# Optimization experiments

Hardware: AMD Instinct MI355X
Metric: run time of the kernel (lower is better)

Reference implementation:

```python
import jax, jax.numpy as jnp
import numpy as np

B, S, D = 1, 2048, 2048
H = 16            # num query heads
QL = 1536         # q_lora_rank
KVL = 512         # kv_lora_rank
DN = 128          # qk_nope_head_dim
DR = 64           # qk_rope_head_dim
DV = 128          # v_head_dim
F = 8192          # ffn intermediate
EPS = 1e-6
WAVE = 10000.0


def _rms(x, scale, eps=EPS):
    # fp32 norm then cast back, matching DeepSeekV3_1RMSNorm
    x32 = x.astype(jnp.float32)
    ms = jnp.mean(x32 * x32, axis=-1, keepdims=True)
    return (x32 * jax.lax.rsqrt(ms + eps)).astype(x.dtype) * scale


def _rope_tables(seq_len, dim):
    inv_freq = 1.0 / (WAVE ** (jnp.arange(0, dim, 2, dtype=jnp.float32) / dim))
    t = jnp.arange(seq_len, dtype=jnp.float32)[:, None] * inv_freq[None, :]  # [S, dim/2]
    emb = jnp.concatenate([t, t], axis=-1)  # [S, dim]
    return jnp.cos(emb), jnp.sin(emb)


def _apply_rope(x, cos, sin):
    # x: [B, S, H, dr]; rotate-half convention
    half = x.shape[-1] // 2
    x1, x2 = x[..., :half], x[..., half:]
    rot = jnp.concatenate([-x2, x1], axis=-1)
    return x * cos[None, :, None, :] + rot * sin[None, :, None, :]


def setup_inputs() -> dict:
    key = jax.random.key(0)
    ks = jax.random.split(key, 12)
    w = lambda k, shp: (jax.random.normal(k, shp, dtype=jnp.float32) * 0.02)
    inp = {
        "hidden_states": jax.random.normal(ks[0], (B, S, D), dtype=jnp.float32),
        "attention_mask": jnp.broadcast_to(jnp.tril(jnp.ones((S, S), dtype=bool)), (B, S, S)),
        "pre_attn_scale": jnp.ones((D,), jnp.float32),
        "wqa": w(ks[1], (D, QL)),
        "q_norm_scale": jnp.ones((QL,), jnp.float32),
        "wqb": w(ks[2], (QL, H * (DN + DR))),
        "wkva": w(ks[3], (D, KVL + DR)),
        "kv_norm_scale": jnp.ones((KVL,), jnp.float32),
        "wkvb": w(ks[4], (KVL, H * (DN + DV))),
        "wo": w(ks[5], (H * DV, D)),
        "pre_ffn_scale": jnp.ones((D,), jnp.float32),
        "wg": w(ks[6], (D, F)),
        "bg": jnp.zeros((F,), jnp.float32),
        "wu": w(ks[7], (D, F)),
        "bu": jnp.zeros((F,), jnp.float32),
        "wd": w(ks[8], (F, D)),
        "bd": jnp.zeros((D,), jnp.float32),
    }
    return inp


def reference(hidden_states, attention_mask, pre_attn_scale, wqa, q_norm_scale, wqb,
              wkva, kv_norm_scale, wkvb, wo, pre_ffn_scale, wg, bg, wu, bu, wd, bd):
    x = hidden_states
    # --- pre-attention RMSNorm ---
    n = _rms(x, pre_attn_scale)
    # --- MLA attention ---
    q = (_rms(n @ wqa, q_norm_scale) @ wqb).reshape(B, S, H, DN + DR)
    q_nope, q_rope = q[..., :DN], q[..., DN:]
    kva = n @ wkva                              # [B,S,KVL+DR]
    c_kv, k_rope = kva[..., :KVL], kva[..., KVL:]
    kv = (_rms(c_kv, kv_norm_scale) @ wkvb).reshape(B, S, H, DN + DV)
    k_nope, v = kv[..., :DN], kv[..., DN:]
    cos, sin = _rope_tables(S, DR)
    q_rope = _apply_rope(q_rope, cos, sin)
    k_rope = _apply_rope(k_rope[:, :, None, :], cos, sin)  # [B,S,1,DR] shared across heads
    qf = jnp.concatenate([q_nope, q_rope], axis=-1)
    kf = jnp.concatenate([k_nope, jnp.broadcast_to(k_rope, (B, S, H, DR))], axis=-1)
    scale = 1.0 / float(np.sqrt(DN + DR))
    scores = jnp.einsum('bqhd,bkhd->bhqk', qf, kf) * scale
    scores = jnp.where(attention_mask[:, None, :, :], scores, jnp.float32(-1e9))
    probs = jax.nn.softmax(scores, axis=-1)
    attn = jnp.einsum('bhqk,bkhd->bqhd', probs, v).reshape(B, S, H * DV)
    x = x + attn @ wo                            # residual 1 (dropout=0)
    # --- pre-FFN RMSNorm + dense SwiGLU FFN ---
    n = _rms(x, pre_ffn_scale)
    ff = (jax.nn.silu(n @ wg + bg) * (n @ wu + bu)) @ wd + bd
    return x + ff                                # residual 2
```

## Files before the change

kernel.cpp:

```cpp
#include <hip/hip_runtime.h>
#include <hip/hip_bf16.h>
#include <stdint.h>

typedef unsigned short u16;
using f32x4  = __attribute__((ext_vector_type(4))) float;
using bf16x8 = __attribute__((ext_vector_type(8))) __bf16;
using u32x4  = __attribute__((ext_vector_type(4))) uint32_t;
using u16x4  = __attribute__((ext_vector_type(4))) unsigned short;
using u16x8  = __attribute__((ext_vector_type(8))) unsigned short;

#define S_LEN 2048
#define DM    2048
#define NH    16
#define QLR   1536
#define KVLR  512
#define DNOPE 128
#define DROPE 64
#define DVAL  128
#define FFD   8192

static __device__ __forceinline__ float bf2f(u16 u) {
    union { uint32_t i; float f; } v; v.i = ((uint32_t)u) << 16; return v.f;
}
static __device__ __forceinline__ u16 f2bf(float f) {
    union { float f; uint32_t i; } v; v.f = f;
    uint32_t x = v.i;
    return (u16)((x + 0x7FFF + ((x >> 16) & 1)) >> 16);
}
static __device__ __forceinline__ void gload16(const u16* g, const u16* l) {
    __builtin_amdgcn_global_load_lds(
        (const __attribute__((address_space(1))) void*)g,
        (__attribute__((address_space(3))) void*)l, 16, 0, 0);
}

__global__ __launch_bounds__(256)
void transpose_w(const float* __restrict__ src, u16* __restrict__ dst, int R, int C)
{
    __shared__ __align__(16) u16 tile[64][68];
    const int c0 = blockIdx.x * 64, r0 = blockIdx.y * 64;
    const int t = threadIdx.x;
#pragma unroll
    for (int i = 0; i < 4; ++i) {
        int idx = i * 256 + t;
        int r = idx >> 4, c4 = idx & 15;
        float4 v = *reinterpret_cast<const float4*>(&src[(size_t)(r0 + r) * C + c0 + c4 * 4]);
        u16x4 b; b[0] = f2bf(v.x); b[1] = f2bf(v.y); b[2] = f2bf(v.z); b[3] = f2bf(v.w);
        *reinterpret_cast<u16x4*>(&tile[r][c4 * 4]) = b;
    }
    __syncthreads();
#pragma unroll
    for (int i = 0; i < 4; ++i) {
        int idx = i * 256 + t;
        int rr = idx >> 4, k4 = idx & 15;
        u16x4 o;
#pragma unroll
        for (int j = 0; j < 4; ++j) o[j] = tile[k4 * 4 + j][rr];
        *reinterpret_cast<u16x4*>(&dst[(size_t)(c0 + rr) * R + r0 + k4 * 4]) = o;
    }
}

__global__ __launch_bounds__(256)
void transpose_v(const u16* __restrict__ kv, u16* __restrict__ vt)
{
    __shared__ __align__(16) u16 tile[64][76];
    const int t = threadIdx.x;
    const int s0 = blockIdx.x * 64;
    const int d0 = blockIdx.y * 64;
    const int h  = blockIdx.z;
#pragma unroll
    for (int i = 0; i < 2; ++i) {
        int idx = i * 256 + t;
        int s = idx >> 3, c8 = idx & 7;
        u16x8 v = *reinterpret_cast<const u16x8*>(kv + (size_t)(s0 + s) * (NH * 256) + h * 256 + 128 + d0 + c8 * 8);
        u16x4 lo, hi;
#pragma unroll
        for (int j = 0; j < 4; ++j) { lo[j] = v[j]; hi[j] = v[4 + j]; }
        *reinterpret_cast<u16x4*>(&tile[s][c8 * 8])     = lo;
        *reinterpret_cast<u16x4*>(&tile[s][c8 * 8 + 4]) = hi;
    }
    __syncthreads();
#pragma unroll
    for (int i = 0; i < 4; ++i) {
        int idx = i * 256 + t;
        int d = idx >> 4, s4 = idx & 15;
        u16x4 o;
#pragma unroll
        for (int j = 0; j < 4; ++j) o[j] = tile[s4 * 4 + j][d];
        *reinterpret_cast<u16x4*>(&vt[(size_t)(h * 128 + d0 + d) * S_LEN + s0 + s4 * 4]) = o;
    }
}

template<bool IN_F32>
__global__ __launch_bounds__(256)
void rms_norm(const void* __restrict__ in, int in_stride, int width,
              const float* __restrict__ scale, u16* __restrict__ out, int out_stride)
{
    const int row = blockIdx.x;
    const int t = threadIdx.x;
    const float* inf = (const float*)in;
    const u16*   inb = (const u16*)in;
    float ss = 0.f;
    for (int c = t; c < width; c += 256) {
        float v = IN_F32 ? inf[(size_t)row * in_stride + c] : bf2f(inb[(size_t)row * in_stride + c]);
        ss += v * v;
    }
#pragma unroll
    for (int o = 32; o > 0; o >>= 1) ss += __shfl_xor(ss, o);
    __shared__ float red[4];
    if ((t & 63) == 0) red[t >> 6] = ss;
    __syncthreads();
    float inv = rsqrtf((red[0] + red[1] + red[2] + red[3]) / (float)width + 1e-6f);
    for (int c = t; c < width; c += 256) {
        float v = IN_F32 ? inf[(size_t)row * in_stride + c] : bf2f(inb[(size_t)row * in_stride + c]);
        out[(size_t)row * out_stride + c] = f2bf(v * inv * scale[c]);
    }
}

__global__ __launch_bounds__(256)
void rope_qk(u16* __restrict__ q, const u16* __restrict__ kva, u16* __restrict__ kr)
{
    const int s = blockIdx.x;
    const int t = threadIdx.x;
    for (int idx = t; idx < 544; idx += 256) {
        int d = idx & 31;
        float invf = powf(10000.f, -(float)(2 * d) / 64.f);
        float ang = (float)s * invf;
        float cs = cosf(ang), sn = sinf(ang);
        if (idx < 512) {
            int hh = idx >> 5;
            u16* base = q + ((size_t)s * NH + hh) * 192 + 128;
            float x1 = bf2f(base[d]), x2 = bf2f(base[d + 32]);
            base[d]      = f2bf(x1 * cs - x2 * sn);
            base[d + 32] = f2bf(x2 * cs + x1 * sn);
        } else {
            const u16* kb = kva + (size_t)s * 576 + 512;
            float x1 = bf2f(kb[d]), x2 = bf2f(kb[d + 32]);
            kr[(size_t)s * 64 + d]      = f2bf(x1 * cs - x2 * sn);
            kr[(size_t)s * 64 + d + 32] = f2bf(x2 * cs + x1 * sn);
        }
    }
}

__global__ __launch_bounds__(256)
void init_out(const float* __restrict__ x2, const float* __restrict__ bd,
              float* __restrict__ out, int total4, int N)
{
    int i = blockIdx.x * 256 + threadIdx.x;
    const int stride = gridDim.x * 256;
    for (; i < total4; i += stride) {
        float4 r = ((const float4*)x2)[i];
        int col = (i * 4) & (N - 1);
        float4 b = *reinterpret_cast<const float4*>(&bd[col]);
        float4 o; o.x = r.x + b.x; o.y = r.y + b.y; o.z = r.z + b.z; o.w = r.w + b.w;
        ((float4*)out)[i] = o;
    }
}

template<int EPI>
__global__ __launch_bounds__(256)
void gemm_bt(const u16* __restrict__ A, const u16* __restrict__ BT,
             void* __restrict__ out, int M, int N, int K)
{
    __shared__ __align__(16) u16 As[128 * 64];
    __shared__ __align__(16) u16 Bs[128 * 64];
    const int t = threadIdx.x;
    const int lane = t & 63;
    const int w = t >> 6;
    const int wr = w >> 1, wc = w & 1;
    const int li = lane & 15;
    const int lg = lane >> 4;

    const int gx = gridDim.x;
    int nwg = gx * gridDim.y;
    int bid = blockIdx.y * gx + blockIdx.x;
    bid = (bid & 7) * (nwg >> 3) + (bid >> 3);
    const int m0 = (bid % gx) * 128;
    const int n0 = (bid / gx) * 128;

    const int srow = w * 32 + (lane >> 3);
    const int scol = (((lane & 7) ^ (lane >> 3)) << 3);
    const u16* ag = A  + (size_t)(m0 + srow) * K + scol;
    const u16* bg = BT + (size_t)(n0 + srow) * K + scol;

    f32x4 acc[4][4];
#pragma unroll
    for (int m = 0; m < 4; ++m)
#pragma unroll
        for (int n = 0; n < 4; ++n)
            acc[m][n] = f32x4{0.f, 0.f, 0.f, 0.f};

    const int nkt = K >> 6;
    for (int kt = 0; kt < nkt; ++kt) {
        const int k0 = kt << 6;
        __syncthreads();
#pragma unroll
        for (int i = 0; i < 4; ++i) {
            gload16(ag + (size_t)i * 8 * K + k0, As + (w * 32 + i * 8) * 64);
            gload16(bg + (size_t)i * 8 * K + k0, Bs + (w * 32 + i * 8) * 64);
        }
        __syncthreads();
#pragma unroll
        for (int kk = 0; kk < 2; ++kk) {
            const int csw = (kk * 32 + lg * 8) ^ ((li & 7) << 3);
            bf16x8 af[4], bfr[4];
#pragma unroll
            for (int m = 0; m < 4; ++m)
                af[m] = *reinterpret_cast<const bf16x8*>(As + (wr * 64 + m * 16 + li) * 64 + csw);
#pragma unroll
            for (int n = 0; n < 4; ++n)
                bfr[n] = *reinterpret_cast<const bf16x8*>(Bs + (wc * 64 + n * 16 + li) * 64 + csw);
#pragma unroll
            for (int m = 0; m < 4; ++m)
#pragma unroll
                for (int n = 0; n < 4; ++n)
                    acc[m][n] = __builtin_amdgcn_mfma_f32_16x16x32_bf16(af[m], bfr[n], acc[m][n], 0, 0, 0);
        }
    }

#pragma unroll
    for (int m = 0; m < 4; ++m) {
        const int row = m0 + wr * 64 + m * 16 + lg * 4;
#pragma unroll
        for (int n = 0; n < 4; ++n) {
            const int col = n0 + wc * 64 + n * 16 + li;
            if (col < N) {
#pragma unroll
                for (int r2 = 0; r2 < 4; ++r2)
                    ((u16*)out)[(size_t)(row + r2) * N + col] = f2bf(acc[m][n][r2]);
            }
        }
    }
}

template<int EPI>
__global__ __launch_bounds__(512, 4)
void gemm_big(const u16* __restrict__ A, const u16* __restrict__ BT,
              void* __restrict__ out, int M, int N, int K,
              const float* __restrict__ bias, const u16* __restrict__ gmul)
{
    __shared__ __align__(16) u16 As[256 * 64];
    __shared__ __align__(16) u16 Bs[128 * 64];
    const int t = threadIdx.x;
    const int lane = t & 63;
    const int w = t >> 6;
    const int wr = w >> 1, wc = w & 1;
    const int li = lane & 15;
    const int lg = lane >> 4;

    const int gx = gridDim.x;
    int nwg = gx * gridDim.y;
    int bid = blockIdx.y * gx + blockIdx.x;
    bid = (bid & 7) * (nwg >> 3) + (bid >> 3);
    const int m0 = (bid % gx) * 256;
    const int n0 = (bid / gx) * 128;

    const int nz = gridDim.z, z = blockIdx.z;
    const int nktt = K >> 6;
    const int qq = nktt / nz, rr = nktt % nz;
    const int kt0 = z * qq + (z < rr ? z : rr);
    const int ktEnd = kt0 + qq + (z < rr ? 1 : 0);

    const int sr = lane >> 3;
    const int scol = (((lane & 7) ^ sr) << 3);
    const u16* ag = A  + (size_t)(m0 + w * 8 + sr) * K + scol;
    const u16* bg = BT + (size_t)(n0 + w * 8 + sr) * K + scol;
    const u16* lA = As + (w * 8) * 64;
    const u16* lB = Bs + (w * 8) * 64;

    f32x4 acc[4][4];
#pragma unroll
    for (int m = 0; m < 4; ++m)
#pragma unroll
        for (int n = 0; n < 4; ++n)
            acc[m][n] = f32x4{0.f, 0.f, 0.f, 0.f};

    for (int kt = kt0; kt < ktEnd; ++kt) {
        const int k0 = kt << 6;
        __syncthreads();
#pragma unroll
        for (int i = 0; i < 4; ++i)
            gload16(ag + (size_t)i * 64 * K + k0, lA + i * 64 * 64);
#pragma unroll
        for (int i = 0; i < 2; ++i)
            gload16(bg + (size_t)i * 64 * K + k0, lB + i * 64 * 64);
        __syncthreads();
        __builtin_amdgcn_s_setprio(1);
#pragma unroll
        for (int kk = 0; kk < 2; ++kk) {
            const int csw = (kk * 32 + lg * 8) ^ ((li & 7) << 3);
            bf16x8 af[4], bfr[4];
#pragma unroll
            for (int m = 0; m < 4; ++m)
                af[m] = *reinterpret_cast<const bf16x8*>(As + (wr * 64 + m * 16 + li) * 64 + csw);
#pragma unroll
            for (int n = 0; n < 4; ++n)
                bfr[n] = *reinterpret_cast<const bf16x8*>(Bs + (wc * 64 + n * 16 + li) * 64 + csw);
#pragma unroll
            for (int m = 0; m < 4; ++m)
#pragma unroll
                for (int n = 0; n < 4; ++n)
                    acc[m][n] = __builtin_amdgcn_mfma_f32_16x16x32_bf16(af[m], bfr[n], acc[m][n], 0, 0, 0);
        }
        __builtin_amdgcn_s_setprio(0);
    }

#pragma unroll
    for (int m = 0; m < 4; ++m) {
        const int row = m0 + wr * 64 + m * 16 + lg * 4;
#pragma unroll
        for (int n = 0; n < 4; ++n) {
            const int col = n0 + wc * 64 + n * 16 + li;
#pragma unroll
            for (int r2 = 0; r2 < 4; ++r2) {
                float v = acc[m][n][r2];
                size_t idx = (size_t)(row + r2) * N + col;
                if (EPI == 0) {
                    ((u16*)out)[idx] = f2bf(v);
                } else if (EPI == 1) {
                    v += bias[col];
                    v = v / (1.f + __expf(-v));
                    ((u16*)out)[idx] = f2bf(v);
                } else if (EPI == 2) {
                    v = (v + bias[col]) * bf2f(gmul[idx]);
                    ((u16*)out)[idx] = f2bf(v);
                } else {
                    unsafeAtomicAdd((float*)out + idx, v);
                }
            }
        }
    }
}

__global__ __launch_bounds__(256)
void flash_attn(const u16* __restrict__ q, const u16* __restrict__ kv,
                const u16* __restrict__ kr, const u16* __restrict__ vt,
                u16* __restrict__ attn)
{
    __shared__ __align__(16) u16 KVs[2][20480];
    __shared__ __align__(16) u16 Ps[4][16][72];

    const int t = threadIdx.x;
    const int lane = t & 63;
    const int w = t >> 6;
    const int li = lane & 15;
    const int lg = lane >> 4;
    const int h = blockIdx.x;
    const int by = blockIdx.y;

    const int qtp[2]  = {31 - by, by};
    const int nktp[2] = {32 - by, by + 1};

    auto stage = [&](int buf, int k0) {
        u16* base = &KVs[buf][0];
#pragma unroll
        for (int i = 0; i < 6; ++i) {
            int g = w * 6 + i;
            int P = g * 64 + lane;
            int j = P / 24, s = P % 24;
            int c = (s & 24) | ((s ^ (j & 7)) & 7);
            const u16* src = (c < 16)
                ? kv + (size_t)(k0 + j) * (NH * 256) + h * 256 + c * 8
                : kr + (size_t)(k0 + j) * 64 + (c - 16) * 8;
            gload16(src, base + g * 512);
        }
#pragma unroll
        for (int i = 0; i < 4; ++i) {
            int g = w * 4 + i;
            int P = g * 64 + lane;
            int d = P >> 3, s8 = P & 7;
            int c = s8 ^ (d & 7);
            const u16* src = vt + (size_t)(h * 128 + d) * S_LEN + k0 + c * 8;
            gload16(src, base + 12288 + g * 512);
        }
    };

    stage(0, 0);
    int buf = 0;
    const float scale = 0.07216878364870322f;

    for (int pass = 0; pass < 2; ++pass) {
        const int qt = qtp[pass];
        const int nkt = nktp[pass];
        const int qr = qt * 64 + w * 16;
        const int qpos = qr + li;

        bf16x8 qf[6];
#pragma unroll
        for (int kb = 0; kb < 6; ++kb)
            qf[kb] = *reinterpret_cast<const bf16x8*>(q + ((size_t)(qr + li) * NH + h) * 192 + kb * 32 + lg * 8);

        f32x4 oacc[8];
#pragma unroll
        for (int i = 0; i < 8; ++i) oacc[i] = f32x4{0.f, 0.f, 0.f, 0.f};
        float m_run = -INFINITY, l_run = 0.f;

        for (int kt = 0; kt < nkt; ++kt) {
            const int k0 = kt << 6;
            __syncthreads();
            if (kt + 1 < nkt)       stage(buf ^ 1, (kt + 1) << 6);
            else if (pass == 0)     stage(buf ^ 1, 0);

            const u16* bb = &KVs[buf][0];

            f32x4 sacc[4];
#pragma unroll
            for (int jt = 0; jt < 4; ++jt) sacc[jt] = f32x4{0.f, 0.f, 0.f, 0.f};
            __builtin_amdgcn_s_setprio(1);
#pragma unroll
            for (int kb = 0; kb < 6; ++kb) {
                const int c = kb * 4 + lg;
                const int s = (c & 24) | ((c ^ (li & 7)) & 7);
#pragma unroll
                for (int jt = 0; jt < 4; ++jt) {
                    bf16x8 kf = *reinterpret_cast<const bf16x8*>(bb + ((jt * 16 + li) * 24 + s) * 8);
                    sacc[jt] = __builtin_amdgcn_mfma_f32_16x16x32_bf16(kf, qf[kb], sacc[jt], 0, 0, 0);
                }
            }
            __builtin_amdgcn_s_setprio(0);

            float p[16];
            float mt = -INFINITY;
            if (k0 + 63 <= qr) {
#pragma unroll
                for (int jt = 0; jt < 4; ++jt)
#pragma unroll
                    for (int r = 0; r < 4; ++r) {
                        float sv = sacc[jt][r] * scale;
                        p[jt * 4 + r] = sv;
                        mt = fmaxf(mt, sv);
                    }
            } else {
#pragma unroll
                for (int jt = 0; jt < 4; ++jt)
#pragma unroll
                    for (int r = 0; r < 4; ++r) {
                        int jpos = k0 + jt * 16 + lg * 4 + r;
                        float sv = (jpos <= qpos) ? sacc[jt][r] * scale : -INFINITY;
                        p[jt * 4 + r] = sv;
                        mt = fmaxf(mt, sv);
                    }
            }
            mt = fmaxf(mt, __shfl_xor(mt, 16));
            mt = fmaxf(mt, __shfl_xor(mt, 32));
            if (!__all(mt <= m_run + 8.f)) {
                float mn = fmaxf(m_run, mt);
                float sf = __expf(m_run - mn);
                float sfr[4];
#pragma unroll
                for (int r = 0; r < 4; ++r)
                    sfr[r] = __shfl(sf, (lane & 48) + lg * 4 + r);
#pragma unroll
                for (int d2 = 0; d2 < 8; ++d2)
#pragma unroll
                    for (int r = 0; r < 4; ++r)
                        oacc[d2][r] *= sfr[r];
                l_run *= sf;
                m_run = mn;
            }
            float rsum = 0.f;
#pragma unroll
            for (int i2 = 0; i2 < 16; ++i2) { p[i2] = __expf(p[i2] - m_run); rsum += p[i2]; }
            rsum += __shfl_xor(rsum, 16);
            rsum += __shfl_xor(rsum, 32);
            l_run += rsum;

#pragma unroll
            for (int jt = 0; jt < 4; ++jt) {
                u16x4 pk;
                pk[0] = f2bf(p[jt * 4 + 0]); pk[1] = f2bf(p[jt * 4 + 1]);
                pk[2] = f2bf(p[jt * 4 + 2]); pk[3] = f2bf(p[jt * 4 + 3]);
                *reinterpret_cast<u16x4*>(&Ps[w][li][jt * 16 + lg * 4]) = pk;
            }

            __builtin_amdgcn_s_setprio(1);
#pragma unroll
            for (int ks = 0; ks < 2; ++ks) {
                bf16x8 pf = *reinterpret_cast<const bf16x8*>(&Ps[w][li][ks * 32 + lg * 8]);
                const int vs = (ks * 4 + lg) ^ (li & 7);
#pragma unroll
                for (int d2 = 0; d2 < 8; ++d2) {
                    bf16x8 vf = *reinterpret_cast<const bf16x8*>(bb + 12288 + ((d2 * 16 + li) * 8 + vs) * 8);
                    oacc[d2] = __builtin_amdgcn_mfma_f32_16x16x32_bf16(pf, vf, oacc[d2], 0, 0, 0);
                }
            }
            __builtin_amdgcn_s_setprio(0);
            buf ^= 1;
        }

        float rl = 1.f / l_run;
        float rlr[4];
#pragma unroll
        for (int r = 0; r < 4; ++r)
            rlr[r] = __shfl(rl, (lane & 48) + lg * 4 + r);
#pragma unroll
        for (int d2 = 0; d2 < 8; ++d2)
#pragma unroll
            for (int r = 0; r < 4; ++r) {
                int srow = qr + lg * 4 + r;
                int dcol = d2 * 16 + li;
                attn[(size_t)srow * (NH * DVAL) + h * DVAL + dcol] = f2bf(oacc[d2][r] * rlr[r]);
            }
    }
}

extern "C" void kernel_launch(void* const* d_in, const int* in_sizes, int n_in,
                              void* d_out, int out_size, void* d_ws, size_t ws_size,
                              hipStream_t stream)
{
    const float* hidden   = (const float*)d_in[0];
    const float* pa_scale = (const float*)d_in[2];
    const float* wqa      = (const float*)d_in[3];
    const float* qn_scale = (const float*)d_in[4];
    const float* wqb      = (const float*)d_in[5];
    const float* wkva     = (const float*)d_in[6];
    const float* kv_scale = (const float*)d_in[7];
    const float* wkvb     = (const float*)d_in[8];
    const float* wo       = (const float*)d_in[9];
    const float* pf_scale = (const float*)d_in[10];
    const float* wg       = (const float*)d_in[11];
    const float* bg       = (const float*)d_in[12];
    const float* wu       = (const float*)d_in[13];
    const float* bu       = (const float*)d_in[14];
    const float* wd       = (const float*)d_in[15];
    const float* bd       = (const float*)d_in[16];
    float* out = (float*)d_out;

    size_t off = 0;
    auto alloc = [&](size_t bytes) {
        off = (off + 255) & ~(size_t)255;
        void* p = (char*)d_ws + off;
        off += bytes;
        return p;
    };
    u16* wqaT  = (u16*)alloc((size_t)QLR * DM * 2);
    u16* wqbT  = (u16*)alloc((size_t)3072 * QLR * 2);
    u16* wkvaT = (u16*)alloc((size_t)640 * DM * 2);
    u16* wkvbT = (u16*)alloc((size_t)4096 * KVLR * 2);
    u16* woT   = (u16*)alloc((size_t)DM * DM * 2);
    u16* wgT   = (u16*)alloc((size_t)FFD * DM * 2);
    u16* wuT   = (u16*)alloc((size_t)FFD * DM * 2);
    u16* wdT   = (u16*)alloc((size_t)DM * FFD * 2);
    u16* n1    = (u16*)alloc((size_t)S_LEN * DM * 2);
    u16* qlora = (u16*)alloc((size_t)S_LEN * QLR * 2);
    u16* qn    = (u16*)alloc((size_t)S_LEN * QLR * 2);
    u16* qbuf  = (u16*)alloc((size_t)S_LEN * 3072 * 2);
    u16* kva   = (u16*)alloc((size_t)S_LEN * 576 * 2);
    u16* ckvn  = (u16*)alloc((size_t)S_LEN * KVLR * 2);
    u16* kvbuf = (u16*)alloc((size_t)S_LEN * 4096 * 2);
    u16* krbuf = (u16*)alloc((size_t)S_LEN * 64 * 2);
    u16* attnb = (u16*)alloc((size_t)S_LEN * DM * 2);
    float* x2  = (float*)alloc((size_t)S_LEN * DM * 4);
    u16* n2    = (u16*)alloc((size_t)S_LEN * DM * 2);
    u16* gbuf  = (u16*)alloc((size_t)S_LEN * FFD * 2);
    u16* hbuf  = (u16*)alloc((size_t)S_LEN * FFD * 2);
    u16* vtb = qlora;
    (void)ws_size; (void)in_sizes; (void)n_in; (void)out_size;

    hipLaunchKernelGGL(transpose_w, dim3(1536/64, 2048/64), 256, 0, stream, wqa,  wqaT,  2048, 1536);
    hipLaunchKernelGGL(transpose_w, dim3(3072/64, 1536/64), 256, 0, stream, wqb,  wqbT,  1536, 3072);
    hipLaunchKernelGGL(transpose_w, dim3( 576/64, 2048/64), 256, 0, stream, wkva, wkvaT, 2048,  576);
    hipLaunchKernelGGL(transpose_w, dim3(4096/64,  512/64), 256, 0, stream, wkvb, wkvbT,  512, 4096);
    hipLaunchKernelGGL(transpose_w, dim3(2048/64, 2048/64), 256, 0, stream, wo,   woT,   2048, 2048);
    hipLaunchKernelGGL(transpose_w, dim3(8192/64, 2048/64), 256, 0, stream, wg,   wgT,   2048, 8192);
    hipLaunchKernelGGL(transpose_w, dim3(8192/64, 2048/64), 256, 0, stream, wu,   wuT,   2048, 8192);
    hipLaunchKernelGGL(transpose_w, dim3(2048/64, 8192/64), 256, 0, stream, wd,   wdT,   8192, 2048);

    hipLaunchKernelGGL((rms_norm<true>),  dim3(S_LEN), 256, 0, stream, hidden, DM, DM, pa_scale, n1, DM);

    hipLaunchKernelGGL((gemm_bt<0>), dim3(16, 12), 256, 0, stream, n1, wqaT, qlora, S_LEN, QLR, DM);
    hipLaunchKernelGGL((gemm_bt<0>), dim3(16,  5), 256, 0, stream, n1, wkvaT, kva, S_LEN, 576, DM);
    hipLaunchKernelGGL((rms_norm<false>), dim3(S_LEN), 256, 0, stream, qlora, QLR, QLR, qn_scale, qn, QLR);
    hipLaunchKernelGGL((gemm_bt<0>), dim3(16, 24), 256, 0, stream, qn, wqbT, qbuf, S_LEN, 3072, QLR);
    hipLaunchKernelGGL((rms_norm<false>), dim3(S_LEN), 256, 0, stream, kva, 576, KVLR, kv_scale, ckvn, KVLR);
    hipLaunchKernelGGL(rope_qk, dim3(S_LEN), 256, 0, stream, qbuf, kva, krbuf);
    hipLaunchKernelGGL((gemm_big<0>), dim3(8, 32), 512, 0, stream, ckvn, wkvbT, kvbuf, S_LEN, 4096, KVLR, nullptr, nullptr);

    hipLaunchKernelGGL(transpose_v, dim3(S_LEN/64, 2, NH), 256, 0, stream, kvbuf, vtb);
    hipLaunchKernelGGL(flash_attn, dim3(NH, 16), 256, 0, stream, qbuf, kvbuf, krbuf, vtb, attnb);

    hipMemcpyAsync(x2, hidden, (size_t)S_LEN * DM * 4, hipMemcpyDeviceToDevice, stream);
    hipLaunchKernelGGL((gemm_big<5>), dim3(8, 16, 4), 512, 0, stream, attnb, woT, x2, S_LEN, DM, DM, nullptr, nullptr);

    hipLaunchKernelGGL((rms_norm<true>), dim3(S_LEN), 256, 0, stream, x2, DM, DM, pf_scale, n2, DM);

    hipLaunchKernelGGL(init_out, dim3(2048), 256, 0, stream, x2, bd, out, S_LEN * DM / 4, DM);
    hipLaunchKernelGGL((gemm_big<1>), dim3(8, 64), 512, 0, stream, n2, wgT, gbuf, S_LEN, FFD, DM, bg, nullptr);
    hipLaunchKernelGGL((gemm_big<2>), dim3(8, 64), 512, 0, stream, n2, wuT, hbuf, S_LEN, FFD, DM, bu, gbuf);
    hipLaunchKernelGGL((gemm_big<5>), dim3(8, 16, 4), 512, 0, stream, hbuf, wdT, out, S_LEN, DM, FFD, nullptr, nullptr);
}
```

Before: 675.6 us.

## Double-buffer gemm_big LDS tiles and merge weight transposes into one launch

gemm_big now keeps two LDS buffers and issues the global-to-LDS loads for tile kt+2 while computing tile kt. It uses explicit vmcnt waits and barriers in place of the load-then-sync pattern, and the occupancy hint drops from 4 to 2 blocks to fit the doubled shared memory. Separately, the eight per-weight transpose launches become one kernel that maps each block to a job table entry, removing launch overhead and tail gaps. The risks are lower occupancy in the GEMM and reliance on exact vmcnt accounting for correctness.

```diff
diff --git a/kernel.cpp b/kernel.cpp
--- a/kernel.cpp
+++ b/kernel.cpp
@@ -33,11 +33,23 @@
         (__attribute__((address_space(3))) void*)l, 16, 0, 0);
 }
 
+struct TWJob { const float* src; u16* dst; int R, C, xt, start; };
+struct TWJobs { TWJob j[8]; };
+
 __global__ __launch_bounds__(256)
-void transpose_w(const float* __restrict__ src, u16* __restrict__ dst, int R, int C)
+void transpose_all(TWJobs jobs)
 {
     __shared__ __align__(16) u16 tile[64][68];
-    const int c0 = blockIdx.x * 64, r0 = blockIdx.y * 64;
+    const int bid = blockIdx.x;
+    int e = 0;
+#pragma unroll
+    for (int i = 1; i < 8; ++i) e = (bid >= jobs.j[i].start) ? i : e;
+    const float* src = jobs.j[e].src;
+    u16* dst = jobs.j[e].dst;
+    const int R = jobs.j[e].R, C = jobs.j[e].C;
+    const int local = bid - jobs.j[e].start;
+    const int c0 = (local % jobs.j[e].xt) * 64;
+    const int r0 = (local / jobs.j[e].xt) * 64;
     const int t = threadIdx.x;
 #pragma unroll
     for (int i = 0; i < 4; ++i) {
@@ -233,13 +245,13 @@
 }
 
 template<int EPI>
-__global__ __launch_bounds__(512, 4)
+__global__ __launch_bounds__(512, 2)
 void gemm_big(const u16* __restrict__ A, const u16* __restrict__ BT,
               void* __restrict__ out, int M, int N, int K,
               const float* __restrict__ bias, const u16* __restrict__ gmul)
 {
-    __shared__ __align__(16) u16 As[256 * 64];
-    __shared__ __align__(16) u16 Bs[128 * 64];
+    __shared__ __align__(16) u16 As[2][256 * 64];
+    __shared__ __align__(16) u16 Bs[2][128 * 64];
     const int t = threadIdx.x;
     const int lane = t & 63;
     const int w = t >> 6;
@@ -264,8 +276,18 @@
     const int scol = (((lane & 7) ^ sr) << 3);
     const u16* ag = A  + (size_t)(m0 + w * 8 + sr) * K + scol;
     const u16* bg = BT + (size_t)(n0 + w * 8 + sr) * K + scol;
-    const u16* lA = As + (w * 8) * 64;
-    const u16* lB = Bs + (w * 8) * 64;
+
+    auto stage = [&](int b, int kt) {
+        const int k0 = kt << 6;
+        u16* lA = &As[b][(w * 8) * 64];
+        u16* lB = &Bs[b][(w * 8) * 64];
+#pragma unroll
+        for (int i = 0; i < 4; ++i)
+            gload16(ag + (size_t)i * 64 * K + k0, lA + i * 64 * 64);
+#pragma unroll
+        for (int i = 0; i < 2; ++i)
+            gload16(bg + (size_t)i * 64 * K + k0, lB + i * 64 * 64);
+    };
 
     f32x4 acc[4][4];
 #pragma unroll
@@ -274,33 +296,42 @@
         for (int n = 0; n < 4; ++n)
             acc[m][n] = f32x4{0.f, 0.f, 0.f, 0.f};
 
+    stage(0, kt0);
+    if (kt0 + 1 < ktEnd) stage(1, kt0 + 1);
+
     for (int kt = kt0; kt < ktEnd; ++kt) {
-        const int k0 = kt << 6;
-        __syncthreads();
-#pragma unroll
-        for (int i = 0; i < 4; ++i)
-            gload16(ag + (size_t)i * 64 * K + k0, lA + i * 64 * 64);
-#pragma unroll
-        for (int i = 0; i < 2; ++i)
-            gload16(bg + (size_t)i * 64 * K + k0, lB + i * 64 * 64);
-        __syncthreads();
-        __builtin_amdgcn_s_setprio(1);
+        const int cur = (kt - kt0) & 1;
+        if (kt + 1 < ktEnd) asm volatile("s_waitcnt vmcnt(6)" ::: "memory");
+        else                asm volatile("s_waitcnt vmcnt(0)" ::: "memory");
+        __builtin_amdgcn_s_barrier();
+        __builtin_amdgcn_sched_barrier(0);
+
+        bf16x8 af[2][4], bfr[2][4];
 #pragma unroll
         for (int kk = 0; kk < 2; ++kk) {
             const int csw = (kk * 32 + lg * 8) ^ ((li & 7) << 3);
-            bf16x8 af[4], bfr[4];
 #pragma unroll
             for (int m = 0; m < 4; ++m)
-                af[m] = *reinterpret_cast<const bf16x8*>(As + (wr * 64 + m * 16 + li) * 64 + csw);
+                af[kk][m] = *reinterpret_cast<const bf16x8*>(&As[cur][(wr * 64 + m * 16 + li) * 64 + csw]);
 #pragma unroll
             for (int n = 0; n < 4; ++n)
-                bfr[n] = *reinterpret_cast<const bf16x8*>(Bs + (wc * 64 + n * 16 + li) * 64 + csw);
+                bfr[kk][n] = *reinterpret_cast<const bf16x8*>(&Bs[cur][(wc * 64 + n * 16 + li) * 64 + csw]);
+        }
+        asm volatile("s_waitcnt lgkmcnt(0)" ::: "memory");
+        __builtin_amdgcn_sched_barrier(0);
+        __builtin_amdgcn_s_barrier();
+        __builtin_amdgcn_sched_barrier(0);
+
+        if (kt + 2 < ktEnd) stage(cur, kt + 2);
+
+        __builtin_amdgcn_s_setprio(1);
+#pragma unroll
+        for (int kk = 0; kk < 2; ++kk)
 #pragma unroll
             for (int m = 0; m < 4; ++m)
 #pragma unroll
                 for (int n = 0; n < 4; ++n)
-                    acc[m][n] = __builtin_amdgcn_mfma_f32_16x16x32_bf16(af[m], bfr[n], acc[m][n], 0, 0, 0);
-        }
+                    acc[m][n] = __builtin_amdgcn_mfma_f32_16x16x32_bf16(af[kk][m], bfr[kk][n], acc[m][n], 0, 0, 0);
         __builtin_amdgcn_s_setprio(0);
     }
 
@@ -556,14 +587,21 @@
     u16* vtb = qlora;
     (void)ws_size; (void)in_sizes; (void)n_in; (void)out_size;
 
-    hipLaunchKernelGGL(transpose_w, dim3(1536/64, 2048/64), 256, 0, stream, wqa,  wqaT,  2048, 1536);
-    hipLaunchKernelGGL(transpose_w, dim3(3072/64, 1536/64), 256, 0, stream, wqb,  wqbT,  1536, 3072);
-    hipLaunchKernelGGL(transpose_w, dim3( 576/64, 2048/64), 256, 0, stream, wkva, wkvaT, 2048,  576);
-    hipLaunchKernelGGL(transpose_w, dim3(4096/64,  512/64), 256, 0, stream, wkvb, wkvbT,  512, 4096);
-    hipLaunchKernelGGL(transpose_w, dim3(2048/64, 2048/64), 256, 0, stream, wo,   woT,   2048, 2048);
-    hipLaunchKernelGGL(transpose_w, dim3(8192/64, 2048/64), 256, 0, stream, wg,   wgT,   2048, 8192);
-    hipLaunchKernelGGL(transpose_w, dim3(8192/64, 2048/64), 256, 0, stream, wu,   wuT,   2048, 8192);
-    hipLaunchKernelGGL(transpose_w, dim3(2048/64, 8192/64), 256, 0, stream, wd,   wdT,   8192, 2048);
+    TWJobs jobs;
+    int startAcc = 0;
+    auto setJob = [&](int i, const float* s, u16* d, int R, int C) {
+        jobs.j[i] = TWJob{s, d, R, C, C / 64, startAcc};
+        startAcc += (C / 64) * (R / 64);
+    };
+    setJob(0, wqa,  wqaT,  2048, 1536);
+    setJob(1, wqb,  wqbT,  1536, 3072);
+    setJob(2, wkva, wkvaT, 2048,  576);
+    setJob(3, wkvb, wkvbT,  512, 4096);
+    setJob(4, wo,   woT,   2048, 2048);
+    setJob(5, wg,   wgT,   2048, 8192);
+    setJob(6, wu,   wuT,   2048, 8192);
+    setJob(7, wd,   wdT,   8192, 2048);
+    hipLaunchKernelGGL(transpose_all, dim3(startAcc), 256, 0, stream, jobs);
 
     hipLaunchKernelGGL((rms_norm<true>),  dim3(S_LEN), 256, 0, stream, hidden, DM, DM, pa_scale, n1, DM);
 
```

Measured after the change: 713.8 us. 1.06x slower.
